# Kernel optimization log

Hardware: AMD Instinct MI355X
Metric: run time of the kernel (lower is better)

Reference implementation:

```python
import jax, jax.numpy as jnp
import numpy as np

DIM = 256
HEADS = 4
DIM_HEAD = 32
HIDDEN = HEADS * DIM_HEAD  # 128
EPS = 1e-5


def setup_inputs() -> dict:
    key = jax.random.key(0)
    ks = jax.random.split(key, 6)
    B, H, W = 16, 64, 64
    x = jax.random.normal(ks[0], (B, DIM, H, W), dtype=jnp.float32)
    # 1x1 conv weights stored as [out_ch, in_ch]
    W_qkv = jax.random.normal(ks[1], (HIDDEN * 3, DIM), dtype=jnp.float32) * 0.02
    W_out = jax.random.normal(ks[2], (DIM, HIDDEN), dtype=jnp.float32) * 0.02
    b_out = jnp.zeros((DIM,), dtype=jnp.float32)
    gamma = jnp.ones((DIM,), dtype=jnp.float32)
    beta = jnp.zeros((DIM,), dtype=jnp.float32)
    return {"x": x, "W_qkv": W_qkv, "W_out": W_out, "b_out": b_out,
            "gamma": gamma, "beta": beta}


def reference(x, W_qkv, W_out, b_out, gamma, beta):
    b, c, h, w = x.shape
    n = h * w
    scale = DIM_HEAD ** -0.5
    # 1x1 conv == channel matmul
    qkv = jnp.einsum('bchw,oc->bohw', x, W_qkv)  # [b, 3*hidden, h, w]
    q, k, v = jnp.split(qkv, 3, axis=1)
    def to_heads(t):
        return t.reshape(b, HEADS, DIM_HEAD, n)  # b h d n
    q = jax.nn.softmax(to_heads(q), axis=-2) * scale  # softmax over d
    k = jax.nn.softmax(to_heads(k), axis=-1)           # softmax over n
    v = to_heads(v)
    # context: [b, h, d, e] — tiny 32x32 per head
    context = jnp.einsum('bhdn,bhen->bhde', k, v)
    out = jnp.einsum('bhde,bhdn->bhen', context, q)  # [b, h, e, n]
    out = out.reshape(b, HIDDEN, h, w)
    # output 1x1 conv with bias
    out = jnp.einsum('bchw,oc->bohw', out, W_out) + b_out[None, :, None, None]
    # GroupNorm(1, dim): normalize over (C,H,W) per sample, per-channel affine
    mean = out.mean(axis=(1, 2, 3), keepdims=True)
    var = out.var(axis=(1, 2, 3), keepdims=True)
    out = (out - mean) * jax.lax.rsqrt(var + EPS)
    return out * gamma[None, :, None, None] + beta[None, :, None, None]
```

## Files before the change

kernel.cpp:

```cpp
#include <hip/hip_runtime.h>

#define NN 4096
#define CIN 256
#define O3 384
#define HID 128
#define NHEAD 4
#define DH 32

typedef float f32x4 __attribute__((ext_vector_type(4)));
typedef _Float16 f16x8 __attribute__((ext_vector_type(8)));
typedef _Float16 f16x4 __attribute__((ext_vector_type(4)));
typedef _Float16 f16x2 __attribute__((ext_vector_type(2)));
typedef __fp16 fp16x2_raw __attribute__((ext_vector_type(2)));

__device__ __forceinline__ f16x2 pkrtz(float a, float b) {
  fp16x2_raw r = __builtin_amdgcn_cvt_pkrtz(a, b);
  return __builtin_bit_cast(f16x2, r);
}

__global__ __launch_bounds__(256) void prep(
    const float* __restrict__ Wqkv, const float* __restrict__ Wout,
    _Float16* __restrict__ WpkA, _Float16* __restrict__ WpkB,
    float* __restrict__ zbase, int nz) {
  const int bid = blockIdx.x, tid = threadIdx.x;
  if (bid < 48) {
    int t = bid * 256 + tid;
    int l = t & 63, mk = t >> 6;
    int k32 = mk & 7, m16 = mk >> 3;
    int row = m16 * 16 + (l & 15), k = k32 * 32 + (l >> 4) * 8;
    const float* s = Wqkv + (size_t)row * CIN + k;
    f16x8 o;
#pragma unroll
    for (int j = 0; j < 8; j++) o[j] = (_Float16)s[j];
    *(f16x8*)(WpkA + (size_t)t * 8) = o;
  } else if (bid < 64) {
    int t = (bid - 48) * 256 + tid;
    int l = t & 63, mk = t >> 6;
    int k32 = mk & 3, m16 = mk >> 2;
    int row = m16 * 16 + (l & 15), k = k32 * 32 + (l >> 4) * 8;
    const float* s = Wout + (size_t)row * HID + k;
    f16x8 o;
#pragma unroll
    for (int j = 0; j < 8; j++) o[j] = (_Float16)s[j];
    *(f16x8*)(WpkB + (size_t)t * 8) = o;
  } else {
    int i = (bid - 64) * 256 + tid;
    if (i < nz) zbase[i] = 0.f;
  }
}

__global__ __launch_bounds__(256) void gemm_qkv(
    const float* __restrict__ X, const _Float16* __restrict__ Wpk,
    _Float16* __restrict__ Yt) {
  __shared__ _Float16 Bs[2][128 * 40];
  const int orig = blockIdx.x;
  const int swz = (orig & 7) * 192 + (orig >> 3);
  const int mt = swz % 3;
  const int nb = swz / 3;
  const int n0 = (nb & 31) << 7;
  const int b  = nb >> 5;
  const float* Xb = X + (size_t)b * CIN * NN;
  _Float16* Yb = Yt + (size_t)b * NN * O3;
  const int tid = threadIdx.x, l = tid & 63, wid = tid >> 6;
  const int wm = (wid >> 1) << 6, wn = (wid & 1) << 6;
  const int fr = l & 15, q = l >> 4;
  const int b_n = (tid & 31) << 2, b_kk = (tid >> 5) << 2;
  const int am16 = mt * 8 + (wm >> 4);
  const int tp = tid & 31;
  const int swz3 = ((tp ^ (tp >> 2)) & 3) << 1;
  const int gw4 = (((tid >> 5) ^ swz3) << 2);
  int roff[4];
#pragma unroll
  for (int fn = 0; fn < 4; fn++) {
    const int R = wn + fn * 16 + fr;
    const int sR = ((R >> 2) ^ (R >> 4)) & 3;
    roff[fn] = R * 40 + ((q ^ sR) << 3);
  }

#define LOADX(dst, t_) do { \
    _Pragma("unroll") \
    for (int r_ = 0; r_ < 4; r_++) \
      dst[r_] = *(const f32x4*)(Xb + (size_t)((t_) * 32 + b_kk + r_) * NN + n0 + b_n); \
  } while (0)
#define LOADAH(dst, t_) do { \
    _Pragma("unroll") \
    for (int fm_ = 0; fm_ < 4; fm_++) \
      dst[fm_] = *(const f16x8*)(Wpk + ((size_t)((am16 + fm_) * 8 + (t_)) * 64 + l) * 8); \
  } while (0)
#define CVTW(buf_, src) do { \
    _Pragma("unroll") \
    for (int j_ = 0; j_ < 4; j_++) { \
      f16x2 p0_ = pkrtz(src[0][j_], src[1][j_]); \
      f16x2 p1_ = pkrtz(src[2][j_], src[3][j_]); \
      *(f16x4*)&Bs[buf_][(b_n + j_) * 40 + gw4] = (f16x4){p0_[0], p0_[1], p1_[0], p1_[1]}; \
    } } while (0)

  f32x4 xr[3][4];
  f16x8 ah[2][4];
  f32x4 acc[4][4];
#pragma unroll
  for (int i = 0; i < 4; i++)
#pragma unroll
    for (int j = 0; j < 4; j++) acc[i][j] = (f32x4){0.f, 0.f, 0.f, 0.f};

  LOADX(xr[0], 0);
  CVTW(0, xr[0]);
  LOADAH(ah[0], 0);
  LOADX(xr[1], 1);
  LOADX(xr[2], 2);
  asm volatile("s_waitcnt lgkmcnt(0)" ::: "memory");
  __builtin_amdgcn_s_barrier();
  __builtin_amdgcn_sched_barrier(0);

#pragma unroll
  for (int t = 0; t < 8; t++) {
    const int cur = t & 1, nxt = cur ^ 1;
    f16x8 bh[4];
#pragma unroll
    for (int fn = 0; fn < 4; fn++)
      bh[fn] = *(const f16x8*)&Bs[cur][roff[fn]];
#pragma unroll
    for (int fm = 0; fm < 4; fm++)
#pragma unroll
      for (int fn = 0; fn < 4; fn++)
        acc[fm][fn] = __builtin_amdgcn_mfma_f32_16x16x32_f16(ah[cur][fm], bh[fn], acc[fm][fn], 0, 0, 0);
    if (t < 7) {
      CVTW(nxt, xr[(t + 1) % 3]);
      LOADAH(ah[nxt], t + 1);
      if (t < 5) LOADX(xr[(t + 3) % 3], t + 3);
    }
    asm volatile("s_waitcnt lgkmcnt(0)" ::: "memory");
    __builtin_amdgcn_s_barrier();
    __builtin_amdgcn_sched_barrier(0);
  }

  _Float16* Ep = &Bs[0][0];
  const int st_n = tid >> 4;
  const int st_m8 = (tid & 15) * 8;
#pragma unroll
  for (int p = 0; p < 2; p++) {
    if ((wid & 1) == p) {
#pragma unroll
      for (int fm = 0; fm < 4; fm++) {
        const int ml = wm + fm * 16 + q * 4;
#pragma unroll
        for (int fn = 0; fn < 4; fn++) {
          const int nl = fn * 16 + fr;
          f16x2 h0 = pkrtz(acc[fm][fn][0], acc[fm][fn][1]);
          f16x2 h1 = pkrtz(acc[fm][fn][2], acc[fm][fn][3]);
          *(f16x4*)&Ep[nl * 132 + ml] = (f16x4){h0[0], h0[1], h1[0], h1[1]};
        }
      }
    }
    __syncthreads();
#pragma unroll
    for (int s = 0; s < 4; s++) {
      const int nl = s * 16 + st_n;
      f16x4 lo = *(const f16x4*)&Ep[nl * 132 + st_m8];
      f16x4 hi = *(const f16x4*)&Ep[nl * 132 + st_m8 + 4];
      f16x8 v = (f16x8){lo[0], lo[1], lo[2], lo[3], hi[0], hi[1], hi[2], hi[3]};
      *(f16x8*)(Yb + (size_t)(n0 + p * 64 + nl) * O3 + mt * 128 + st_m8) = v;
    }
    if (p == 0) __syncthreads();
  }
#undef LOADX
#undef LOADAH
#undef CVTW
}

__global__ __launch_bounds__(256) void attn1(
    const _Float16* __restrict__ qkvt, float* __restrict__ ctx_raw,
    float* __restrict__ srow_raw) {
  const int h = blockIdx.x, b = blockIdx.y, ns = blockIdx.z;
  const _Float16* base = qkvt + (size_t)b * NN * O3;
  const _Float16* Kb = base + HID + h * DH;
  const _Float16* Vb = base + 2 * HID + h * DH;
  float* ctx = ctx_raw + (size_t)(b * NHEAD + h) * (DH * DH);
  float* srow = srow_raw + (size_t)(b * NHEAD + h) * DH;
  __shared__ __align__(16) float Es[64][36];
  __shared__ __align__(16) float Vs[64][36];
  __shared__ float ctxs[DH][DH + 1];
  __shared__ float srow_s[DH];
  const int tid = threadIdx.x, l = tid & 63, w = tid >> 6;
  const int d4 = (l >> 3) << 2, e4 = (l & 7) << 2;
  if (tid < DH) srow_s[tid] = 0.f;
  for (int i = tid; i < DH * (DH + 1); i += 256) (&ctxs[0][0])[i] = 0.f;
  float sacc[4] = {0.f, 0.f, 0.f, 0.f};
  float acc[4][4];
#pragma unroll
  for (int i = 0; i < 4; i++)
#pragma unroll
    for (int j = 0; j < 4; j++) acc[i][j] = 0.f;

  for (int c = 0; c < 8; c++) {
    const int n0 = ns * 512 + c * 64;
    const size_t roff = (size_t)(n0 + l) * O3 + w * 8;
    f16x8 kv = *(const f16x8*)(Kb + roff);
    f16x8 vv = *(const f16x8*)(Vb + roff);
    __syncthreads();
    float4 e0, e1, v0, v1;
    e0.x = __expf((float)kv[0]); e0.y = __expf((float)kv[1]);
    e0.z = __expf((float)kv[2]); e0.w = __expf((float)kv[3]);
    e1.x = __expf((float)kv[4]); e1.y = __expf((float)kv[5]);
    e1.z = __expf((float)kv[6]); e1.w = __expf((float)kv[7]);
    v0.x = (float)vv[0]; v0.y = (float)vv[1]; v0.z = (float)vv[2]; v0.w = (float)vv[3];
    v1.x = (float)vv[4]; v1.y = (float)vv[5]; v1.z = (float)vv[6]; v1.w = (float)vv[7];
    *(float4*)&Es[l][w * 8] = e0;
    *(float4*)&Es[l][w * 8 + 4] = e1;
    *(float4*)&Vs[l][w * 8] = v0;
    *(float4*)&Vs[l][w * 8 + 4] = v1;
    __syncthreads();
#pragma unroll
    for (int it = 0; it < 16; it++) {
      const int n = w + 4 * it;
      float ka[4], va[4];
      *(float4*)ka = *(const float4*)&Es[n][d4];
      *(float4*)va = *(const float4*)&Vs[n][e4];
#pragma unroll
      for (int i = 0; i < 4; i++) {
        sacc[i] += ka[i];
#pragma unroll
        for (int j = 0; j < 4; j++) acc[i][j] = fmaf(ka[i], va[j], acc[i][j]);
      }
    }
  }
  if ((l & 7) == 0) {
#pragma unroll
    for (int i = 0; i < 4; i++) atomicAdd(&srow_s[d4 + i], sacc[i]);
  }
#pragma unroll
  for (int i = 0; i < 4; i++)
#pragma unroll
    for (int j = 0; j < 4; j++) atomicAdd(&ctxs[d4 + i][e4 + j], acc[i][j]);
  __syncthreads();
  for (int i = tid; i < DH * DH; i += 256) atomicAdd(&ctx[i], ctxs[i >> 5][i & 31]);
  if (tid < DH) atomicAdd(&srow[tid], srow_s[tid]);
}

__global__ __launch_bounds__(256) void attn2(
    _Float16* __restrict__ qkvt, const float* __restrict__ ctx_raw,
    const float* __restrict__ srow_raw) {
  const int ns = blockIdx.x, h = blockIdx.y, b = blockIdx.z;
  const float* cg = ctx_raw + (size_t)(b * NHEAD + h) * (DH * DH);
  const float* sr = srow_raw + (size_t)(b * NHEAD + h) * DH;
  __shared__ float ctxs[DH][DH + 1];
  const int tid = threadIdx.x;
  for (int i = tid; i < DH * DH; i += 256) ctxs[i >> 5][i & 31] = cg[i] / sr[i >> 5];
  __syncthreads();
  const int n = ns * 256 + tid;
  _Float16* qp = qkvt + ((size_t)b * NN + n) * O3 + h * DH;
  float qv[DH];
#pragma unroll
  for (int i = 0; i < 4; i++) {
    f16x8 v = *(const f16x8*)(qp + i * 8);
#pragma unroll
    for (int j = 0; j < 8; j++) qv[i * 8 + j] = (float)v[j];
  }
  float m = -1e30f;
#pragma unroll
  for (int d = 0; d < DH; d++) m = fmaxf(m, qv[d]);
  float s = 0.f;
#pragma unroll
  for (int d = 0; d < DH; d++) { qv[d] = __expf(qv[d] - m); s += qv[d]; }
  float inv = 0.17677669529663687f / s;
#pragma unroll
  for (int d = 0; d < DH; d++) qv[d] *= inv;
#pragma unroll
  for (int eo = 0; eo < 4; eo++) {
    float o[8];
#pragma unroll
    for (int j = 0; j < 8; j++) o[j] = 0.f;
#pragma unroll
    for (int d = 0; d < DH; d++) {
      float qd = qv[d];
#pragma unroll
      for (int j = 0; j < 8; j++) o[j] = fmaf(ctxs[d][eo * 8 + j], qd, o[j]);
    }
    f16x2 h0 = pkrtz(o[0], o[1]);
    f16x2 h1 = pkrtz(o[2], o[3]);
    f16x2 h2 = pkrtz(o[4], o[5]);
    f16x2 h3 = pkrtz(o[6], o[7]);
    f16x8 ov = (f16x8){h0[0], h0[1], h1[0], h1[1], h2[0], h2[1], h3[0], h3[1]};
    *(f16x8*)(qp + eo * 8) = ov;
  }
}

__global__ __launch_bounds__(256) void proj_stats(
    const _Float16* __restrict__ At, const _Float16* __restrict__ Wpk,
    const float* __restrict__ bias, double* __restrict__ stats) {
  __shared__ _Float16 Bs[128][40];
  const int mt = blockIdx.x;
  const int n0 = blockIdx.y * 128;
  const int b = blockIdx.z;
  const _Float16* Ab = At + (size_t)b * NN * O3;
  const int tid = threadIdx.x, l = tid & 63, wid = tid >> 6;
  const int wm = (wid >> 1) << 6, wn = (wid & 1) << 6;
  const int fr = l & 15, q = l >> 4, kq = q << 3;
  const int am16 = mt * 8 + (wm >> 4);
  const int sr0 = tid >> 2, sc = (tid & 3) << 3;

  f32x4 acc[4][4];
#pragma unroll
  for (int i = 0; i < 4; i++)
#pragma unroll
    for (int j = 0; j < 4; j++) acc[i][j] = (f32x4){0.f, 0.f, 0.f, 0.f};

  for (int k0 = 0; k0 < HID; k0 += 32) {
    f16x8 v0 = *(const f16x8*)(Ab + (size_t)(n0 + sr0) * O3 + k0 + sc);
    f16x8 v1 = *(const f16x8*)(Ab + (size_t)(n0 + 64 + sr0) * O3 + k0 + sc);
    f16x8 ah[4];
#pragma unroll
    for (int fm = 0; fm < 4; fm++)
      ah[fm] = *(const f16x8*)(Wpk + ((size_t)((am16 + fm) * 4 + (k0 >> 5)) * 64 + l) * 8);
    __syncthreads();
    *(f16x8*)&Bs[sr0][sc] = v0;
    *(f16x8*)&Bs[64 + sr0][sc] = v1;
    __syncthreads();
    f16x8 bh[4];
#pragma unroll
    for (int fn = 0; fn < 4; fn++)
      bh[fn] = *(const f16x8*)&Bs[wn + fn * 16 + fr][kq];
#pragma unroll
    for (int fm = 0; fm < 4; fm++)
#pragma unroll
      for (int fn = 0; fn < 4; fn++)
        acc[fm][fn] = __builtin_amdgcn_mfma_f32_16x16x32_f16(ah[fm], bh[fn], acc[fm][fn], 0, 0, 0);
  }
  float lsum = 0.f, lsq = 0.f;
#pragma unroll
  for (int fm = 0; fm < 4; fm++) {
    int rowb = mt * 128 + wm + fm * 16 + q * 4;
#pragma unroll
    for (int r = 0; r < 4; r++) {
      float bv = bias[rowb + r];
#pragma unroll
      for (int fn = 0; fn < 4; fn++) {
        float v = acc[fm][fn][r] + bv;
        lsum += v;
        lsq += v * v;
      }
    }
  }
  double ds = (double)lsum, dq = (double)lsq;
#pragma unroll
  for (int off = 32; off; off >>= 1) {
    ds += __shfl_down(ds, off);
    dq += __shfl_down(dq, off);
  }
  __shared__ double sred[8];
  if (l == 0) { sred[wid] = ds; sred[4 + wid] = dq; }
  __syncthreads();
  if (tid == 0) {
    atomicAdd(&stats[b * 2 + 0], sred[0] + sred[1] + sred[2] + sred[3]);
    atomicAdd(&stats[b * 2 + 1], sred[4] + sred[5] + sred[6] + sred[7]);
  }
}

__global__ __launch_bounds__(256) void proj_write(
    const _Float16* __restrict__ At, const _Float16* __restrict__ Wpk,
    const float* __restrict__ bias, float* __restrict__ out,
    const double* __restrict__ stats, const float* __restrict__ gamma,
    const float* __restrict__ beta) {
  __shared__ _Float16 Bs[128][40];
  const int mt = blockIdx.x;
  const int n0 = blockIdx.y * 128;
  const int b = blockIdx.z;
  const _Float16* Ab = At + (size_t)b * NN * O3;
  float* outb = out + (size_t)b * CIN * NN;
  const int tid = threadIdx.x, l = tid & 63, wid = tid >> 6;
  const int wm = (wid >> 1) << 6, wn = (wid & 1) << 6;
  const int fr = l & 15, q = l >> 4, kq = q << 3;
  const int am16 = mt * 8 + (wm >> 4);
  const int sr0 = tid >> 2, sc = (tid & 3) << 3;

  const double nels = (double)CIN * (double)NN;
  double S = stats[b * 2 + 0], Q2 = stats[b * 2 + 1];
  double mu = S / nels;
  double var = Q2 / nels - mu * mu;
  const float mean = (float)mu;
  const float rstd = (float)rsqrt(var + 1e-5);

  f32x4 acc[4][4];
#pragma unroll
  for (int i = 0; i < 4; i++)
#pragma unroll
    for (int j = 0; j < 4; j++) acc[i][j] = (f32x4){0.f, 0.f, 0.f, 0.f};

  for (int k0 = 0; k0 < HID; k0 += 32) {
    f16x8 v0 = *(const f16x8*)(Ab + (size_t)(n0 + sr0) * O3 + k0 + sc);
    f16x8 v1 = *(const f16x8*)(Ab + (size_t)(n0 + 64 + sr0) * O3 + k0 + sc);
    f16x8 ah[4];
#pragma unroll
    for (int fm = 0; fm < 4; fm++)
      ah[fm] = *(const f16x8*)(Wpk + ((size_t)((am16 + fm) * 4 + (k0 >> 5)) * 64 + l) * 8);
    __syncthreads();
    *(f16x8*)&Bs[sr0][sc] = v0;
    *(f16x8*)&Bs[64 + sr0][sc] = v1;
    __syncthreads();
    f16x8 bh[4];
#pragma unroll
    for (int fn = 0; fn < 4; fn++)
      bh[fn] = *(const f16x8*)&Bs[wn + fn * 16 + fr][kq];
#pragma unroll
    for (int fm = 0; fm < 4; fm++)
#pragma unroll
      for (int fn = 0; fn < 4; fn++)
        acc[fm][fn] = __builtin_amdgcn_mfma_f32_16x16x32_f16(ah[fm], bh[fn], acc[fm][fn], 0, 0, 0);
  }
#pragma unroll
  for (int fm = 0; fm < 4; fm++) {
    int rowb = mt * 128 + wm + fm * 16 + q * 4;
#pragma unroll
    for (int r = 0; r < 4; r++) {
      int row = rowb + r;
      float bv = bias[row];
      float g = gamma[row] * rstd, bt = beta[row];
      float* dst = outb + (size_t)row * NN + n0 + wn + fr;
#pragma unroll
      for (int fn = 0; fn < 4; fn++) {
        float v = acc[fm][fn][r] + bv;
        dst[fn * 16] = (v - mean) * g + bt;
      }
    }
  }
}

extern "C" void kernel_launch(void* const* d_in, const int* in_sizes, int n_in,
                              void* d_out, int out_size, void* d_ws, size_t ws_size,
                              hipStream_t stream) {
  const float* x     = (const float*)d_in[0];
  const float* Wqkv  = (const float*)d_in[1];
  const float* Wout  = (const float*)d_in[2];
  const float* bout  = (const float*)d_in[3];
  const float* gamma = (const float*)d_in[4];
  const float* beta  = (const float*)d_in[5];
  float* out = (float*)d_out;

  char* ws = (char*)d_ws;
  _Float16* qkvt = (_Float16*)ws;
  size_t off = (size_t)16 * NN * O3 * 2;
  _Float16* WpkA = (_Float16*)(ws + off); off += 48 * 256 * 8 * 2;
  _Float16* WpkB = (_Float16*)(ws + off); off += 16 * 256 * 8 * 2;
  float* ctxg = (float*)(ws + off); off += (size_t)16 * NHEAD * DH * DH * 4;
  float* srow = (float*)(ws + off); off += (size_t)16 * NHEAD * DH * 4;
  double* stats = (double*)(ws + off);

  const int nz = 16 * NHEAD * DH * DH + 16 * NHEAD * DH + 64;
  prep<<<64 + (nz + 255) / 256, 256, 0, stream>>>(Wqkv, Wout, WpkA, WpkB, ctxg, nz);
  gemm_qkv<<<dim3(1536), 256, 0, stream>>>(x, WpkA, qkvt);
  attn1<<<dim3(NHEAD, 16, 8), 256, 0, stream>>>(qkvt, ctxg, srow);
  attn2<<<dim3(16, NHEAD, 16), 256, 0, stream>>>(qkvt, ctxg, srow);
  proj_stats<<<dim3(2, 32, 16), 256, 0, stream>>>(qkvt, WpkB, bout, stats);
  proj_write<<<dim3(2, 32, 16), 256, 0, stream>>>(qkvt, WpkB, bout, out, stats, gamma, beta);
}
```

Baseline: 120.0 us.

## Fuse K/V context reduction into QKV GEMM epilogue and drop attn1 kernel

The QKV GEMM's M-tiles are remapped so that tiles 1 and 2 each hold the K and V rows for two heads. Instead of writing K and V to global memory, these blocks compute exp(K)·V^T and the exp-sums directly from the shared-memory epilogue tile, then reduce them with atomics into the context buffers. This removes the separate attn1 kernel launch, along with the K/V store and reload through global memory. In exchange the GEMM epilogue gets longer, with scalar FMA loops and shared and global atomics, and K/V are no longer stored in qkvt.

```diff
diff --git a/kernel.cpp b/kernel.cpp
--- a/kernel.cpp
+++ b/kernel.cpp
@@ -51,7 +51,8 @@
 
 __global__ __launch_bounds__(256) void gemm_qkv(
     const float* __restrict__ X, const _Float16* __restrict__ Wpk,
-    _Float16* __restrict__ Yt) {
+    _Float16* __restrict__ Yt, float* __restrict__ ctx_raw,
+    float* __restrict__ srow_raw) {
   __shared__ _Float16 Bs[2][128 * 40];
   const int orig = blockIdx.x;
   const int swz = (orig & 7) * 192 + (orig >> 3);
@@ -65,7 +66,7 @@
   const int wm = (wid >> 1) << 6, wn = (wid & 1) << 6;
   const int fr = l & 15, q = l >> 4;
   const int b_n = (tid & 31) << 2, b_kk = (tid >> 5) << 2;
-  const int am16 = mt * 8 + (wm >> 4);
+  const int am16 = (mt == 0) ? (wm >> 4) : (8 + (mt - 1) * 4 + (wm ? 8 : 0));
   const int tp = tid & 31;
   const int swz3 = ((tp ^ (tp >> 2)) & 3) << 1;
   const int gw4 = (((tid >> 5) ^ swz3) << 2);
@@ -135,106 +136,105 @@
   }
 
   _Float16* Ep = &Bs[0][0];
-  const int st_n = tid >> 4;
-  const int st_m8 = (tid & 15) * 8;
-#pragma unroll
-  for (int p = 0; p < 2; p++) {
-    if ((wid & 1) == p) {
-#pragma unroll
-      for (int fm = 0; fm < 4; fm++) {
-        const int ml = wm + fm * 16 + q * 4;
-#pragma unroll
-        for (int fn = 0; fn < 4; fn++) {
-          const int nl = fn * 16 + fr;
-          f16x2 h0 = pkrtz(acc[fm][fn][0], acc[fm][fn][1]);
-          f16x2 h1 = pkrtz(acc[fm][fn][2], acc[fm][fn][3]);
-          *(f16x4*)&Ep[nl * 132 + ml] = (f16x4){h0[0], h0[1], h1[0], h1[1]};
+  if (mt == 0) {
+    const int st_n = tid >> 4;
+    const int st_m8 = (tid & 15) * 8;
+#pragma unroll
+    for (int p = 0; p < 2; p++) {
+      if ((wid & 1) == p) {
+#pragma unroll
+        for (int fm = 0; fm < 4; fm++) {
+          const int ml = wm + fm * 16 + q * 4;
+#pragma unroll
+          for (int fn = 0; fn < 4; fn++) {
+            const int nl = fn * 16 + fr;
+            f16x2 h0 = pkrtz(acc[fm][fn][0], acc[fm][fn][1]);
+            f16x2 h1 = pkrtz(acc[fm][fn][2], acc[fm][fn][3]);
+            *(f16x4*)&Ep[nl * 132 + ml] = (f16x4){h0[0], h0[1], h1[0], h1[1]};
+          }
         }
       }
-    }
-    __syncthreads();
-#pragma unroll
-    for (int s = 0; s < 4; s++) {
-      const int nl = s * 16 + st_n;
-      f16x4 lo = *(const f16x4*)&Ep[nl * 132 + st_m8];
-      f16x4 hi = *(const f16x4*)&Ep[nl * 132 + st_m8 + 4];
-      f16x8 v = (f16x8){lo[0], lo[1], lo[2], lo[3], hi[0], hi[1], hi[2], hi[3]};
-      *(f16x8*)(Yb + (size_t)(n0 + p * 64 + nl) * O3 + mt * 128 + st_m8) = v;
-    }
-    if (p == 0) __syncthreads();
+      __syncthreads();
+#pragma unroll
+      for (int s = 0; s < 4; s++) {
+        const int nl = s * 16 + st_n;
+        f16x4 lo = *(const f16x4*)&Ep[nl * 132 + st_m8];
+        f16x4 hi = *(const f16x4*)&Ep[nl * 132 + st_m8 + 4];
+        f16x8 v = (f16x8){lo[0], lo[1], lo[2], lo[3], hi[0], hi[1], hi[2], hi[3]};
+        *(f16x8*)(Yb + (size_t)(n0 + p * 64 + nl) * O3 + st_m8) = v;
+      }
+      if (p == 0) __syncthreads();
+    }
+  } else {
+    const int hl = wid >> 1;
+    const int nbase = (wid & 1) << 5;
+    const int d4 = (l >> 3) << 2, e4 = (l & 7) << 2;
+    float cacc[4][4];
+    float sacc2[4] = {0.f, 0.f, 0.f, 0.f};
+#pragma unroll
+    for (int i = 0; i < 4; i++)
+#pragma unroll
+      for (int j = 0; j < 4; j++) cacc[i][j] = 0.f;
+
+#pragma unroll
+    for (int p = 0; p < 2; p++) {
+      if ((wid & 1) == p) {
+#pragma unroll
+        for (int fm = 0; fm < 4; fm++) {
+          const int ml = wm + fm * 16 + q * 4;
+#pragma unroll
+          for (int fn = 0; fn < 4; fn++) {
+            const int nl = fn * 16 + fr;
+            f16x2 h0 = pkrtz(acc[fm][fn][0], acc[fm][fn][1]);
+            f16x2 h1 = pkrtz(acc[fm][fn][2], acc[fm][fn][3]);
+            *(f16x4*)&Ep[nl * 132 + ml] = (f16x4){h0[0], h0[1], h1[0], h1[1]};
+          }
+        }
+      }
+      __syncthreads();
+      for (int it = 0; it < 32; ++it) {
+        const int nl = nbase + it;
+        f16x4 kx = *(const f16x4*)&Ep[nl * 132 + hl * 32 + d4];
+        f16x4 vx = *(const f16x4*)&Ep[nl * 132 + 64 + hl * 32 + e4];
+        float ke[4], vf[4];
+#pragma unroll
+        for (int i = 0; i < 4; i++) ke[i] = __expf((float)kx[i]);
+#pragma unroll
+        for (int j = 0; j < 4; j++) vf[j] = (float)vx[j];
+#pragma unroll
+        for (int i = 0; i < 4; i++) {
+          sacc2[i] += ke[i];
+#pragma unroll
+          for (int j = 0; j < 4; j++) cacc[i][j] = fmaf(ke[i], vf[j], cacc[i][j]);
+        }
+      }
+      __syncthreads();
+    }
+    float* red = (float*)&Bs[0][0];
+    for (int i = tid; i < 2 * 32 * 33 + 2 * 32; i += 256) red[i] = 0.f;
+    __syncthreads();
+    float* ch = red + hl * (32 * 33);
+#pragma unroll
+    for (int i = 0; i < 4; i++)
+#pragma unroll
+      for (int j = 0; j < 4; j++) atomicAdd(&ch[(d4 + i) * 33 + e4 + j], cacc[i][j]);
+    if (e4 == 0) {
+#pragma unroll
+      for (int i = 0; i < 4; i++) atomicAdd(&red[2112 + hl * 32 + d4 + i], sacc2[i]);
+    }
+    __syncthreads();
+    const int hb = (mt - 1) * 2;
+    float* cg = ctx_raw + ((size_t)b * NHEAD + hb) * (DH * DH);
+    float* sg = srow_raw + ((size_t)b * NHEAD + hb) * DH;
+    for (int i = tid; i < 2 * DH * DH; i += 256) {
+      const int h_l = i >> 10, idx = i & 1023;
+      atomicAdd(&cg[h_l * DH * DH + idx], red[h_l * 1056 + (idx >> 5) * 33 + (idx & 31)]);
+    }
+    if (tid < 2 * DH) atomicAdd(&sg[tid], red[2112 + tid]);
   }
 #undef LOADX
 #undef LOADAH
 #undef CVTW
-}
-
-__global__ __launch_bounds__(256) void attn1(
-    const _Float16* __restrict__ qkvt, float* __restrict__ ctx_raw,
-    float* __restrict__ srow_raw) {
-  const int h = blockIdx.x, b = blockIdx.y, ns = blockIdx.z;
-  const _Float16* base = qkvt + (size_t)b * NN * O3;
-  const _Float16* Kb = base + HID + h * DH;
-  const _Float16* Vb = base + 2 * HID + h * DH;
-  float* ctx = ctx_raw + (size_t)(b * NHEAD + h) * (DH * DH);
-  float* srow = srow_raw + (size_t)(b * NHEAD + h) * DH;
-  __shared__ __align__(16) float Es[64][36];
-  __shared__ __align__(16) float Vs[64][36];
-  __shared__ float ctxs[DH][DH + 1];
-  __shared__ float srow_s[DH];
-  const int tid = threadIdx.x, l = tid & 63, w = tid >> 6;
-  const int d4 = (l >> 3) << 2, e4 = (l & 7) << 2;
-  if (tid < DH) srow_s[tid] = 0.f;
-  for (int i = tid; i < DH * (DH + 1); i += 256) (&ctxs[0][0])[i] = 0.f;
-  float sacc[4] = {0.f, 0.f, 0.f, 0.f};
-  float acc[4][4];
-#pragma unroll
-  for (int i = 0; i < 4; i++)
-#pragma unroll
-    for (int j = 0; j < 4; j++) acc[i][j] = 0.f;
-
-  for (int c = 0; c < 8; c++) {
-    const int n0 = ns * 512 + c * 64;
-    const size_t roff = (size_t)(n0 + l) * O3 + w * 8;
-    f16x8 kv = *(const f16x8*)(Kb + roff);
-    f16x8 vv = *(const f16x8*)(Vb + roff);
-    __syncthreads();
-    float4 e0, e1, v0, v1;
-    e0.x = __expf((float)kv[0]); e0.y = __expf((float)kv[1]);
-    e0.z = __expf((float)kv[2]); e0.w = __expf((float)kv[3]);
-    e1.x = __expf((float)kv[4]); e1.y = __expf((float)kv[5]);
-    e1.z = __expf((float)kv[6]); e1.w = __expf((float)kv[7]);
-    v0.x = (float)vv[0]; v0.y = (float)vv[1]; v0.z = (float)vv[2]; v0.w = (float)vv[3];
-    v1.x = (float)vv[4]; v1.y = (float)vv[5]; v1.z = (float)vv[6]; v1.w = (float)vv[7];
-    *(float4*)&Es[l][w * 8] = e0;
-    *(float4*)&Es[l][w * 8 + 4] = e1;
-    *(float4*)&Vs[l][w * 8] = v0;
-    *(float4*)&Vs[l][w * 8 + 4] = v1;
-    __syncthreads();
-#pragma unroll
-    for (int it = 0; it < 16; it++) {
-      const int n = w + 4 * it;
-      float ka[4], va[4];
-      *(float4*)ka = *(const float4*)&Es[n][d4];
-      *(float4*)va = *(const float4*)&Vs[n][e4];
-#pragma unroll
-      for (int i = 0; i < 4; i++) {
-        sacc[i] += ka[i];
-#pragma unroll
-        for (int j = 0; j < 4; j++) acc[i][j] = fmaf(ka[i], va[j], acc[i][j]);
-      }
-    }
-  }
-  if ((l & 7) == 0) {
-#pragma unroll
-    for (int i = 0; i < 4; i++) atomicAdd(&srow_s[d4 + i], sacc[i]);
-  }
-#pragma unroll
-  for (int i = 0; i < 4; i++)
-#pragma unroll
-    for (int j = 0; j < 4; j++) atomicAdd(&ctxs[d4 + i][e4 + j], acc[i][j]);
-  __syncthreads();
-  for (int i = tid; i < DH * DH; i += 256) atomicAdd(&ctx[i], ctxs[i >> 5][i & 31]);
-  if (tid < DH) atomicAdd(&srow[tid], srow_s[tid]);
 }
 
 __global__ __launch_bounds__(256) void attn2(
@@ -447,8 +447,7 @@
 
   const int nz = 16 * NHEAD * DH * DH + 16 * NHEAD * DH + 64;
   prep<<<64 + (nz + 255) / 256, 256, 0, stream>>>(Wqkv, Wout, WpkA, WpkB, ctxg, nz);
-  gemm_qkv<<<dim3(1536), 256, 0, stream>>>(x, WpkA, qkvt);
-  attn1<<<dim3(NHEAD, 16, 8), 256, 0, stream>>>(qkvt, ctxg, srow);
+  gemm_qkv<<<dim3(1536), 256, 0, stream>>>(x, WpkA, qkvt, ctxg, srow);
   attn2<<<dim3(16, NHEAD, 16), 256, 0, stream>>>(qkvt, ctxg, srow);
   proj_stats<<<dim3(2, 32, 16), 256, 0, stream>>>(qkvt, WpkB, bout, stats);
   proj_write<<<dim3(2, 32, 16), 256, 0, stream>>>(qkvt, WpkB, bout, out, stats, gamma, beta);
```

Result: slower. 135.5 us (+12.9%).
